# Optimization experiments

Hardware: AMD Instinct MI355X
Metric: run time of the kernel (lower is better)

Reference implementation:

```python
import jax, jax.numpy as jnp
import numpy as np

K = 16  # neighbors (module's self.k)


def _gather(points, idx):
    # points (B,C,N), idx (B,M[,k]) -> (B,C,M[,k])
    return jax.vmap(lambda p, i: p[:, i])(points, idx)


def _fps(xyz, nsample):
    # furthest point sampling on xyz (B,3,N) -> idx (B,nsample) int32
    B, _, N = xyz.shape

    def body(carry, _):
        dists, last = carry
        lp = jnp.take_along_axis(xyz, last[:, None, None], axis=2)  # (B,3,1)
        d = jnp.sum((xyz - lp) ** 2, axis=1)  # (B,N)
        dists = jnp.minimum(dists, d)
        nxt = jnp.argmax(dists, axis=1).astype(jnp.int32)
        return (dists, nxt), nxt

    init_idx = jnp.zeros((B,), dtype=jnp.int32)
    init_d = jnp.full((B, N), jnp.finfo(xyz.dtype).max, xyz.dtype)
    _, rest = jax.lax.scan(body, (init_d, init_idx), None, length=nsample - 1)
    return jnp.concatenate([init_idx[None], rest], axis=0).T  # (B,nsample)


def _knn(query, points, k):
    # query (B,C,M), points (B,C,N): k nearest in feature space
    d = (jnp.sum(query ** 2, axis=1)[:, :, None]
         + jnp.sum(points ** 2, axis=1)[:, None, :]
         - 2.0 * jnp.einsum('bcm,bcn->bmn', query, points))  # (B,M,N)
    _, idx = jax.lax.top_k(-d, k)  # (B,M,k)
    return _gather(points, idx), idx  # (B,C,M,k), (B,M,k)


def _conv1x1(W, b, y):
    # y (B,Cin,M,k), W (Cout,Cin) -> (B,Cout,M,k)
    return jnp.einsum('oi,bimk->bomk', W, y) + b[None, :, None, None]


def setup_inputs() -> dict:
    key = jax.random.key(0)
    ks = jax.random.split(key, 8)
    B, C, N = 4, 64, 8192
    g = 64
    return {
        'x': jax.random.normal(ks[0], (B, C, N), jnp.float32),
        'xyz': jax.random.normal(ks[1], (B, 3, N), jnp.float32),
        'W0': jax.random.normal(ks[2], (g, 2 * C), jnp.float32) * 0.05,
        'b0': jax.random.normal(ks[3], (g,), jnp.float32) * 0.05,
        'W1': jax.random.normal(ks[4], (g, C + g), jnp.float32) * 0.05,
        'b1': jax.random.normal(ks[5], (g,), jnp.float32) * 0.05,
        'W2': jax.random.normal(ks[6], (g, C + 2 * g), jnp.float32) * 0.05,
        'b2': jax.random.normal(ks[7], (g,), jnp.float32) * 0.05,
        'nsample': 2048,
    }


def reference(x, xyz, W0, b0, W1, b1, W2, b2, nsample):
    # furthest point sample on coordinates, gather sampled features
    sampled_idx = _fps(xyz, nsample)              # (B,M)
    sampled_xyz = _gather(xyz, sampled_idx)       # (B,3,M)
    sampled_x = _gather(x, sampled_idx)           # (B,C,M)
    # local graph: k+1 NN in feature space, drop self
    knn_pt, _ = _knn(sampled_x, x, K + 1)
    knn_pt = knn_pt[..., 1:]                      # (B,C,M,K)
    center = sampled_x[..., None]                 # (B,C,M,1)
    center_k = jnp.broadcast_to(center, knn_pt.shape)
    edge = jnp.concatenate([center_k, knn_pt - center_k], axis=1)  # (B,2C,M,K)
    # dense edge conv cascade
    y = jnp.concatenate([jax.nn.relu(_conv1x1(W0, b0, edge)), center_k], axis=1)
    y = jnp.concatenate([jax.nn.relu(_conv1x1(W1, b1, y)), y], axis=1)
    y = jnp.concatenate([_conv1x1(W2, b2, y), y], axis=1)
    y = jnp.max(y, axis=-1)                       # (B, C+3*g, M)
    return (y, sampled_xyz, sampled_idx)
```

## Files before the change

kernel.cpp:

```cpp
#include <hip/hip_runtime.h>
#include <hip/hip_bf16.h>
#include <stdint.h>

typedef unsigned long long u64;
typedef unsigned int u32;
typedef unsigned short u16;

#define B_   4
#define C_   64
#define N_   8192
#define M_   2048
#define KNB  16
#define FLT_MAX_ 3.402823466e+38f

__device__ __forceinline__ int clampN(int v) {
    return v < 0 ? 0 : (v > N_ - 1 ? N_ - 1 : v);
}


__device__ __forceinline__ void pin4(float4& v) {
    asm volatile("" : "+v"(v.x), "+v"(v.y), "+v"(v.z), "+v"(v.w));
}

__device__ __forceinline__ float wave_fmax_dpp(float v) {
    float t;
    t = __int_as_float(__builtin_amdgcn_update_dpp(0, __float_as_int(v), 0x111, 0xf, 0xf, true)); v = fmaxf(v, t);
    t = __int_as_float(__builtin_amdgcn_update_dpp(0, __float_as_int(v), 0x112, 0xf, 0xf, true)); v = fmaxf(v, t);
    t = __int_as_float(__builtin_amdgcn_update_dpp(0, __float_as_int(v), 0x114, 0xf, 0xf, true)); v = fmaxf(v, t);
    t = __int_as_float(__builtin_amdgcn_update_dpp(0, __float_as_int(v), 0x118, 0xf, 0xf, true)); v = fmaxf(v, t);
    t = __int_as_float(__builtin_amdgcn_update_dpp(0, __float_as_int(v), 0x142, 0xa, 0xf, true)); v = fmaxf(v, t);
    t = __int_as_float(__builtin_amdgcn_update_dpp(0, __float_as_int(v), 0x143, 0xc, 0xf, true)); v = fmaxf(v, t);
    return __int_as_float(__builtin_amdgcn_readlane(__float_as_int(v), 63));
}

#define FPS_STEP(PX, PY, PZ, DD, J)                                          \
    {                                                                        \
        float dx = __fsub_rn((PX), lx);                                      \
        float dy = __fsub_rn((PY), ly);                                      \
        float dz = __fsub_rn((PZ), lz);                                      \
        float d = __fadd_rn(__fadd_rn(__fmul_rn(dx, dx), __fmul_rn(dy, dy)), \
                            __fmul_rn(dz, dz));                              \
        float nd = fminf((DD), d);                                           \
        (DD) = nd;                                                           \
        bool gt = nd > fm;                                                   \
        fm = gt ? nd : fm;                                                   \
        fj = gt ? (J) : fj;                                                  \
        fx = gt ? (PX) : fx;                                                 \
        fy = gt ? (PY) : fy;                                                 \
        fz = gt ? (PZ) : fz;                                                 \
    }

__global__ __launch_bounds__(512, 2) void fps_prep_kernel(
    const float* __restrict__ xyz, const float* __restrict__ x,
    const float* __restrict__ W0, const float* __restrict__ W1,
    const float* __restrict__ W2, u16* __restrict__ idx_ws,
    float* __restrict__ pnorm_ws, float* __restrict__ wt,
    float* __restrict__ out1, float* __restrict__ out2) {
    const int bid = blockIdx.x;
    const int tid = threadIdx.x;

    __shared__ float4 red4[2][8];
    __shared__ int    redi[2][8];
    __shared__ u16    hist[M_];

    if (bid >= 64) {
        if (bid < 128) {
            int gid = (bid - 64) * 512 + tid;
            int b = gid >> 13, n = gid & 8191;
            const float* xb = x + b * C_ * N_ + n;
            float acc = 0.f;
#pragma unroll 16
            for (int c = 0; c < C_; ++c) { float v = xb[c * N_]; acc = fmaf(v, v, acc); }
            pnorm_ws[gid] = acc;
        } else {
            int e = (bid - 128) * 512 + tid;
            if (e < 8192) {
                int i = e >> 6, o = e & 63;
                wt[e] = W0[o * 128 + i];
            } else if (e < 16384) {
                int e2 = e - 8192; int i = e2 >> 6, o = e2 & 63;
                wt[8192 + e2] = W1[o * 128 + i];
            } else {
                int e2 = e - 16384; int i = e2 >> 6, o = e2 & 63;
                wt[16384 + e2] = W2[o * 192 + i];
            }
        }
        return;
    }

    const int rep = bid >> 2;
    const int b = bid & 3;
    const int lane = tid & 63;
    const int w = tid >> 6;
    const float* xb = xyz + b * 3 * N_;
    const int n0 = tid * 16;

    float4 px[4], py[4], pz[4], dd[4];
#pragma unroll
    for (int j4 = 0; j4 < 4; ++j4) {
        px[j4] = *(const float4*)(xb + n0 + j4 * 4);
        py[j4] = *(const float4*)(xb + N_ + n0 + j4 * 4);
        pz[j4] = *(const float4*)(xb + 2 * N_ + n0 + j4 * 4);
        pin4(px[j4]); pin4(py[j4]); pin4(pz[j4]);
        dd[j4] = make_float4(FLT_MAX_, FLT_MAX_, FLT_MAX_, FLT_MAX_);
    }

    int cur = 0;
    float lx = xb[0], ly = xb[N_], lz = xb[2 * N_];
    if (tid == 0) { idx_ws[b * M_ + 0] = 0; hist[0] = 0; }

    for (int s = 1; s < M_; ++s) {
        float fm = -1.0f, fx = 0.f, fy = 0.f, fz = 0.f;
        int fj = 0;
#pragma unroll
        for (int j4 = 0; j4 < 4; ++j4) {
            FPS_STEP(px[j4].x, py[j4].x, pz[j4].x, dd[j4].x, j4 * 4 + 0);
            FPS_STEP(px[j4].y, py[j4].y, pz[j4].y, dd[j4].y, j4 * 4 + 1);
            FPS_STEP(px[j4].z, py[j4].z, pz[j4].z, dd[j4].z, j4 * 4 + 2);
            FPS_STEP(px[j4].w, py[j4].w, pz[j4].w, dd[j4].w, j4 * 4 + 3);
        }
        float wm = wave_fmax_dpp(fm);
        u64 bal = __ballot(fm == wm);
        int winlane = (int)__ffsll(bal) - 1;
        const int par = s & 1;
        if (lane == winlane) {
            red4[par][w] = make_float4(wm, fx, fy, fz);
            redi[par][w] = n0 + fj;
        }
        __syncthreads();
        float4 p0 = red4[par][0];
        float g = p0.x; float nlx = p0.y, nly = p0.z, nlz = p0.w;
        int ncur = redi[par][0];
#pragma unroll
        for (int ww = 1; ww < 8; ++ww) {
            float4 p = red4[par][ww];
            int id = redi[par][ww];
            bool gt = p.x > g;
            g = gt ? p.x : g;
            nlx = gt ? p.y : nlx; nly = gt ? p.z : nly; nlz = gt ? p.w : nlz;
            ncur = gt ? id : ncur;
        }
        lx = nlx; ly = nly; lz = nlz; cur = ncur;
        if (tid == 0) { idx_ws[b * M_ + s] = (u16)cur; hist[s] = (u16)cur; }
    }

    __syncthreads();
    if (rep == 0) {
        for (int m = tid; m < M_; m += 512) {
            int idx = (int)hist[m];
            out2[b * M_ + m] = (float)idx;
            out1[(b * 3 + 0) * M_ + m] = xb[idx];
            out1[(b * 3 + 1) * M_ + m] = xb[N_ + idx];
            out1[(b * 3 + 2) * M_ + m] = xb[2 * N_ + idx];
        }
    }
}

__global__ __launch_bounds__(256) void knn_kernel(const float* __restrict__ x,
                                                  const u16* __restrict__ idx_ws,
                                                  const float* __restrict__ pnorm_ws,
                                                  u16* __restrict__ nbr_ws) {
    __shared__ float pt[64 * 68];
    __shared__ float spn[64];
    __shared__ u64 lists[256 * 17];

    const int tid = threadIdx.x;
    const int b = blockIdx.x >> 6;
    const int m0 = (blockIdx.x & 63) * 32;
    const int q = tid & 31, sub = tid >> 5;
    const int m = m0 + q;
    const float* xb = x + b * C_ * N_;
    const int self = clampN((int)idx_ws[b * M_ + m]);

    float4 qv[16];
#pragma unroll
    for (int c4 = 0; c4 < 16; ++c4) {
        qv[c4].x = xb[(c4 * 4 + 0) * N_ + self];
        qv[c4].y = xb[(c4 * 4 + 1) * N_ + self];
        qv[c4].z = xb[(c4 * 4 + 2) * N_ + self];
        qv[c4].w = xb[(c4 * 4 + 3) * N_ + self];
    }
    const float qn = pnorm_ws[b * N_ + self];

    u64* L = lists + tid * 17;
#pragma unroll
    for (int j = 0; j < 17; ++j) L[j] = ~0ULL;
    u64 worst = ~0ULL;

    for (int t = 0; t < N_ / 64; ++t) {
        const int nb0 = t * 64;
        __syncthreads();
#pragma unroll
        for (int r = 0; r < 4; ++r) {
            int e = tid + r * 256;
            int c = e >> 4, nq = e & 15;
            float4 v = *(const float4*)(xb + c * N_ + nb0 + nq * 4);
            const int cs = c ^ (nq << 2);
            pt[(nq * 4 + 0) * 68 + cs] = v.x;
            pt[(nq * 4 + 1) * 68 + cs] = v.y;
            pt[(nq * 4 + 2) * 68 + cs] = v.z;
            pt[(nq * 4 + 3) * 68 + cs] = v.w;
        }
        if (tid < 64) spn[tid] = pnorm_ws[b * N_ + nb0 + tid];
        __syncthreads();
#pragma unroll
        for (int pp = 0; pp < 8; ++pp) {
            int nl = sub * 8 + pp;
            const float* pvbase = pt + nl * 68;
            const int rsw = (nl >> 2) << 2;
            float a0 = 0.f, a1 = 0.f, a2 = 0.f, a3 = 0.f;
#pragma unroll
            for (int c4 = 0; c4 < 16; ++c4) {
                float4 p = *(const float4*)(pvbase + (((c4 << 2) ^ rsw)));
                a0 = fmaf(qv[c4].x, p.x, a0);
                a1 = fmaf(qv[c4].y, p.y, a1);
                a2 = fmaf(qv[c4].z, p.z, a2);
                a3 = fmaf(qv[c4].w, p.w, a3);
            }
            float dot = (a0 + a1) + (a2 + a3);
            float d = qn + spn[nl] - 2.0f * dot;
            u32 db = __float_as_uint(d);
            db = (db & 0x80000000u) ? ~db : (db | 0x80000000u);
            u64 key = ((u64)db << 32) | (u32)(nb0 + nl);
            if (key < worst) {
                int j = 16;
                while (j > 0 && L[j - 1] > key) { L[j] = L[j - 1]; --j; }
                L[j] = key;
                worst = L[16];
            }
        }
    }
    __syncthreads();
    if (tid < 32) {
        int pos[8];
#pragma unroll
        for (int s2 = 0; s2 < 8; ++s2) pos[s2] = 0;
        u16* outp = nbr_ws + (b * M_ + m0 + tid) * KNB;
        for (int r = 0; r < 17; ++r) {
            u64 best = ~0ULL; int bs = 0;
#pragma unroll
            for (int s2 = 0; s2 < 8; ++s2) {
                u64 k2 = (pos[s2] < 17) ? lists[(tid + 32 * s2) * 17 + pos[s2]] : ~0ULL;
                if (k2 < best) { best = k2; bs = s2; }
            }
#pragma unroll
            for (int s2 = 0; s2 < 8; ++s2) pos[s2] += (s2 == bs) ? 1 : 0;
            if (r > 0) outp[r - 1] = (u16)clampN((int)(best & 0xFFFFFFFFu));
        }
    }
}

__device__ __forceinline__ void mm_tile(float a[4][4], const float* __restrict__ w,
                                        const float* __restrict__ s, int ni) {
#pragma unroll 8
    for (int i = 0; i < ni; ++i) {
        const float4 w4 = *(const float4*)(w + i * 64);
        const float4 e4 = *(const float4*)(s + i * 64);
        a[0][0] = fmaf(w4.x, e4.x, a[0][0]);
        a[0][1] = fmaf(w4.x, e4.y, a[0][1]);
        a[0][2] = fmaf(w4.x, e4.z, a[0][2]);
        a[0][3] = fmaf(w4.x, e4.w, a[0][3]);
        a[1][0] = fmaf(w4.y, e4.x, a[1][0]);
        a[1][1] = fmaf(w4.y, e4.y, a[1][1]);
        a[1][2] = fmaf(w4.y, e4.z, a[1][2]);
        a[1][3] = fmaf(w4.y, e4.w, a[1][3]);
        a[2][0] = fmaf(w4.z, e4.x, a[2][0]);
        a[2][1] = fmaf(w4.z, e4.y, a[2][1]);
        a[2][2] = fmaf(w4.z, e4.z, a[2][2]);
        a[2][3] = fmaf(w4.z, e4.w, a[2][3]);
        a[3][0] = fmaf(w4.w, e4.x, a[3][0]);
        a[3][1] = fmaf(w4.w, e4.y, a[3][1]);
        a[3][2] = fmaf(w4.w, e4.z, a[3][2]);
        a[3][3] = fmaf(w4.w, e4.w, a[3][3]);
    }
}

__global__ __launch_bounds__(256) void conv_kernel(const float* __restrict__ x,
                                                   const u16* __restrict__ idx_ws,
                                                   const u16* __restrict__ nbr_ws,
                                                   const float* __restrict__ wt,
                                                   const float* __restrict__ bias0,
                                                   const float* __restrict__ bias1,
                                                   const float* __restrict__ bias2,
                                                   float* __restrict__ out0) {
    __shared__ float E[128 * 64];
    __shared__ float H0[64 * 64];

    const int tid = threadIdx.x;
    const int b = blockIdx.x >> 9;
    const int m0 = (blockIdx.x & 511) * 4;
    const float* xb = x + b * C_ * N_;

    {
        const int col = tid & 63;
        const int half = tid >> 6;
        const int m = m0 + (col >> 4);
        const int k = col & 15;
        const int selfm = clampN((int)idx_ws[b * M_ + m]);
        const int nbr = clampN((int)nbr_ws[(b * M_ + m) * KNB + k]);
#pragma unroll
        for (int c2 = 0; c2 < 16; ++c2) {
            int c = half * 16 + c2;
            float ctr = xb[c * N_ + selfm];
            float nb = xb[c * N_ + nbr];
            E[c * 64 + col] = ctr;
            E[(64 + c) * 64 + col] = __fsub_rn(nb, ctr);
        }
    }
    __syncthreads();

    const int o0 = (tid >> 4) * 4;
    const int c0 = (tid & 15) * 4;
    float a[4][4];

    {
        float4 bb = *(const float4*)(bias0 + o0);
        a[0][0] = a[0][1] = a[0][2] = a[0][3] = bb.x;
        a[1][0] = a[1][1] = a[1][2] = a[1][3] = bb.y;
        a[2][0] = a[2][1] = a[2][2] = a[2][3] = bb.z;
        a[3][0] = a[3][1] = a[3][2] = a[3][3] = bb.w;
        mm_tile(a, wt + o0, E + c0, 128);
#pragma unroll
        for (int oo = 0; oo < 4; ++oo) {
            float4 v = make_float4(fmaxf(a[oo][0], 0.f), fmaxf(a[oo][1], 0.f),
                                   fmaxf(a[oo][2], 0.f), fmaxf(a[oo][3], 0.f));
            *(float4*)(H0 + (o0 + oo) * 64 + c0) = v;
        }
    }
    __syncthreads();

    {
        float4 bb = *(const float4*)(bias1 + o0);
        a[0][0] = a[0][1] = a[0][2] = a[0][3] = bb.x;
        a[1][0] = a[1][1] = a[1][2] = a[1][3] = bb.y;
        a[2][0] = a[2][1] = a[2][2] = a[2][3] = bb.z;
        a[3][0] = a[3][1] = a[3][2] = a[3][3] = bb.w;
        mm_tile(a, wt + 8192 + o0, H0 + c0, 64);
        mm_tile(a, wt + 8192 + 64 * 64 + o0, E + c0, 64);
#pragma unroll
        for (int oo = 0; oo < 4; ++oo) {
            float4 v = make_float4(fmaxf(a[oo][0], 0.f), fmaxf(a[oo][1], 0.f),
                                   fmaxf(a[oo][2], 0.f), fmaxf(a[oo][3], 0.f));
            *(float4*)(E + (64 + o0 + oo) * 64 + c0) = v;
        }
    }
    __syncthreads();

    {
        float4 bb = *(const float4*)(bias2 + o0);
        a[0][0] = a[0][1] = a[0][2] = a[0][3] = bb.x;
        a[1][0] = a[1][1] = a[1][2] = a[1][3] = bb.y;
        a[2][0] = a[2][1] = a[2][2] = a[2][3] = bb.z;
        a[3][0] = a[3][1] = a[3][2] = a[3][3] = bb.w;
        mm_tile(a, wt + 16384 + o0, E + 64 * 64 + c0, 64);
        mm_tile(a, wt + 16384 + 64 * 64 + o0, H0 + c0, 64);
        mm_tile(a, wt + 16384 + 128 * 64 + o0, E + c0, 64);
    }

#pragma unroll
    for (int r = 1; r < 4; ++r) {
        int e = tid + r * 256;
        int ch = e >> 2, mloc = e & 3;
        int colb = mloc * 16;
        float v;
        if (ch < 128) {
            const float* row = E + (64 + (ch - 64)) * 64 + colb;
            v = row[0];
#pragma unroll
            for (int k = 1; k < 16; ++k) v = fmaxf(v, row[k]);
        } else if (ch < 192) {
            const float* row = H0 + (ch - 128) * 64 + colb;
            v = row[0];
#pragma unroll
            for (int k = 1; k < 16; ++k) v = fmaxf(v, row[k]);
        } else {
            v = E[(ch - 192) * 64 + colb];
        }
        out0[((b * 256 + ch) << 11) + m0 + mloc] = v;
    }
    __syncthreads();

    {
#pragma unroll
        for (int oo = 0; oo < 4; ++oo) {
            float4 v = make_float4(a[oo][0], a[oo][1], a[oo][2], a[oo][3]);
            *(float4*)(E + (64 + o0 + oo) * 64 + c0) = v;
        }
    }
    __syncthreads();

    {
        int e = tid;
        int ch = e >> 2, mloc = e & 3;
        int colb = mloc * 16;
        const float* row = E + (64 + ch) * 64 + colb;
        float v = row[0];
#pragma unroll
        for (int k = 1; k < 16; ++k) v = fmaxf(v, row[k]);
        out0[((b * 256 + ch) << 11) + m0 + mloc] = v;
    }
}

extern "C" void kernel_launch(void* const* d_in, const int* in_sizes, int n_in,
                              void* d_out, int out_size, void* d_ws, size_t ws_size,
                              hipStream_t stream) {
    const float* x   = (const float*)d_in[0];
    const float* xyz = (const float*)d_in[1];
    const float* W0  = (const float*)d_in[2];
    const float* b0  = (const float*)d_in[3];
    const float* W1  = (const float*)d_in[4];
    const float* b1  = (const float*)d_in[5];
    const float* W2  = (const float*)d_in[6];
    const float* b2  = (const float*)d_in[7];

    float* out  = (float*)d_out;
    float* out0 = out;
    float* out1 = out + 4 * 256 * 2048;
    float* out2 = out1 + 4 * 3 * 2048;

    char* ws = (char*)d_ws;
    u16*   idx_ws   = (u16*)ws;
    u16*   nbr_ws   = (u16*)(ws + 16384);
    float* pnorm_ws = (float*)(ws + 278528);
    float* wt_ws    = (float*)(ws + 409600);

    fps_prep_kernel<<<184, 512, 0, stream>>>(xyz, x, W0, W1, W2,
                                             idx_ws, pnorm_ws, wt_ws, out1, out2);
    knn_kernel<<<256, 256, 0, stream>>>(x, idx_ws, pnorm_ws, nbr_ws);
    conv_kernel<<<2048, 256, 0, stream>>>(x, idx_ws, nbr_ws, wt_ws, b0, b1, b2, out0);
}
```

Before: 2.969 ms.

## Fuse FPS and KNN into one persistent kernel with flag-based streaming

Measured after the change: 3.432 ms. 1.16x slower.

```diff
diff --git a/kernel.cpp b/kernel.cpp
--- a/kernel.cpp
+++ b/kernel.cpp
@@ -12,6 +12,7 @@
 #define M_   2048
 #define KNB  16
 #define FLT_MAX_ 3.402823466e+38f
+#define SMEM_SZ 86016
 
 __device__ __forceinline__ int clampN(int v) {
     return v < 0 ? 0 : (v > N_ - 1 ? N_ - 1 : v);
@@ -50,202 +51,227 @@
         fz = gt ? (PZ) : fz;                                                 \
     }
 
-__global__ __launch_bounds__(512, 2) void fps_prep_kernel(
+__global__ void init_kernel(u32* __restrict__ flags) {
+    if (threadIdx.x < 16) flags[threadIdx.x] = 0;
+}
+
+__global__ __launch_bounds__(256, 1) void mega_kernel(
     const float* __restrict__ xyz, const float* __restrict__ x,
     const float* __restrict__ W0, const float* __restrict__ W1,
     const float* __restrict__ W2, u16* __restrict__ idx_ws,
     float* __restrict__ pnorm_ws, float* __restrict__ wt,
-    float* __restrict__ out1, float* __restrict__ out2) {
+    float* __restrict__ out1, float* __restrict__ out2,
+    u16* __restrict__ nbr_ws, u32* __restrict__ flags) {
     const int bid = blockIdx.x;
     const int tid = threadIdx.x;
-
-    __shared__ float4 red4[2][8];
-    __shared__ int    redi[2][8];
-    __shared__ u16    hist[M_];
-
-    if (bid >= 64) {
-        if (bid < 128) {
-            int gid = (bid - 64) * 512 + tid;
-            int b = gid >> 13, n = gid & 8191;
-            const float* xb = x + b * C_ * N_ + n;
-            float acc = 0.f;
-#pragma unroll 16
-            for (int c = 0; c < C_; ++c) { float v = xb[c * N_]; acc = fmaf(v, v, acc); }
-            pnorm_ws[gid] = acc;
-        } else {
-            int e = (bid - 128) * 512 + tid;
-            if (e < 8192) {
-                int i = e >> 6, o = e & 63;
-                wt[e] = W0[o * 128 + i];
-            } else if (e < 16384) {
-                int e2 = e - 8192; int i = e2 >> 6, o = e2 & 63;
-                wt[8192 + e2] = W1[o * 128 + i];
-            } else {
-                int e2 = e - 16384; int i = e2 >> 6, o = e2 & 63;
-                wt[16384 + e2] = W2[o * 192 + i];
-            }
-        }
-        return;
-    }
-
-    const int rep = bid >> 2;
-    const int b = bid & 3;
-    const int lane = tid & 63;
-    const int w = tid >> 6;
-    const float* xb = xyz + b * 3 * N_;
-    const int n0 = tid * 16;
-
-    float4 px[4], py[4], pz[4], dd[4];
-#pragma unroll
-    for (int j4 = 0; j4 < 4; ++j4) {
-        px[j4] = *(const float4*)(xb + n0 + j4 * 4);
-        py[j4] = *(const float4*)(xb + N_ + n0 + j4 * 4);
-        pz[j4] = *(const float4*)(xb + 2 * N_ + n0 + j4 * 4);
-        pin4(px[j4]); pin4(py[j4]); pin4(pz[j4]);
-        dd[j4] = make_float4(FLT_MAX_, FLT_MAX_, FLT_MAX_, FLT_MAX_);
-    }
-
-    int cur = 0;
-    float lx = xb[0], ly = xb[N_], lz = xb[2 * N_];
-    if (tid == 0) { idx_ws[b * M_ + 0] = 0; hist[0] = 0; }
-
-    for (int s = 1; s < M_; ++s) {
-        float fm = -1.0f, fx = 0.f, fy = 0.f, fz = 0.f;
-        int fj = 0;
-#pragma unroll
-        for (int j4 = 0; j4 < 4; ++j4) {
-            FPS_STEP(px[j4].x, py[j4].x, pz[j4].x, dd[j4].x, j4 * 4 + 0);
-            FPS_STEP(px[j4].y, py[j4].y, pz[j4].y, dd[j4].y, j4 * 4 + 1);
-            FPS_STEP(px[j4].z, py[j4].z, pz[j4].z, dd[j4].z, j4 * 4 + 2);
-            FPS_STEP(px[j4].w, py[j4].w, pz[j4].w, dd[j4].w, j4 * 4 + 3);
-        }
-        float wm = wave_fmax_dpp(fm);
-        u64 bal = __ballot(fm == wm);
-        int winlane = (int)__ffsll(bal) - 1;
-        const int par = s & 1;
-        if (lane == winlane) {
-            red4[par][w] = make_float4(wm, fx, fy, fz);
-            redi[par][w] = n0 + fj;
-        }
+    __shared__ __align__(16) char SM[SMEM_SZ];
+
+    if (bid < 4) {
+        const int b = bid;
+        const int lane = tid & 63;
+        const int w = tid >> 6;
+        const float* xb = xyz + b * 3 * N_;
+        const int n0 = tid * 32;
+
+        float4* red4 = (float4*)SM;
+        int*    redi = (int*)(SM + 128);
+        u16*    hist = (u16*)(SM + 160);
+
+        float4 px[8], py[8], pz[8], dd[8];
+#pragma unroll
+        for (int j4 = 0; j4 < 8; ++j4) {
+            px[j4] = *(const float4*)(xb + n0 + j4 * 4);
+            py[j4] = *(const float4*)(xb + N_ + n0 + j4 * 4);
+            pz[j4] = *(const float4*)(xb + 2 * N_ + n0 + j4 * 4);
+            pin4(px[j4]); pin4(py[j4]); pin4(pz[j4]);
+            dd[j4] = make_float4(FLT_MAX_, FLT_MAX_, FLT_MAX_, FLT_MAX_);
+        }
+
+        int cur = 0;
+        float lx = xb[0], ly = xb[N_], lz = xb[2 * N_];
+        if (tid == 0) { idx_ws[b * M_ + 0] = 0; hist[0] = 0; }
+
+        for (int s = 1; s < M_; ++s) {
+            float fm = -1.0f, fx = 0.f, fy = 0.f, fz = 0.f;
+            int fj = 0;
+#pragma unroll
+            for (int j4 = 0; j4 < 8; ++j4) {
+                FPS_STEP(px[j4].x, py[j4].x, pz[j4].x, dd[j4].x, j4 * 4 + 0);
+                FPS_STEP(px[j4].y, py[j4].y, pz[j4].y, dd[j4].y, j4 * 4 + 1);
+                FPS_STEP(px[j4].z, py[j4].z, pz[j4].z, dd[j4].z, j4 * 4 + 2);
+                FPS_STEP(px[j4].w, py[j4].w, pz[j4].w, dd[j4].w, j4 * 4 + 3);
+            }
+            float wm = wave_fmax_dpp(fm);
+            u64 bal = __ballot(fm == wm);
+            int winlane = (int)__ffsll(bal) - 1;
+            const int par = s & 1;
+            if (lane == winlane) {
+                red4[(par << 2) + w] = make_float4(wm, fx, fy, fz);
+                redi[(par << 2) + w] = n0 + fj;
+            }
+            __syncthreads();
+            float4 p0 = red4[par << 2];
+            float g = p0.x; float nlx = p0.y, nly = p0.z, nlz = p0.w;
+            int ncur = redi[par << 2];
+#pragma unroll
+            for (int ww = 1; ww < 4; ++ww) {
+                float4 p = red4[(par << 2) + ww];
+                int id = redi[(par << 2) + ww];
+                bool gt = p.x > g;
+                g = gt ? p.x : g;
+                nlx = gt ? p.y : nlx; nly = gt ? p.z : nly; nlz = gt ? p.w : nlz;
+                ncur = gt ? id : ncur;
+            }
+            lx = nlx; ly = nly; lz = nlz; cur = ncur;
+            if (tid == 0) {
+                idx_ws[b * M_ + s] = (u16)cur; hist[s] = (u16)cur;
+                if ((s & 63) == 63)
+                    __hip_atomic_store(&flags[b], (u32)s, __ATOMIC_RELEASE,
+                                       __HIP_MEMORY_SCOPE_AGENT);
+            }
+        }
+
         __syncthreads();
-        float4 p0 = red4[par][0];
-        float g = p0.x; float nlx = p0.y, nly = p0.z, nlz = p0.w;
-        int ncur = redi[par][0];
-#pragma unroll
-        for (int ww = 1; ww < 8; ++ww) {
-            float4 p = red4[par][ww];
-            int id = redi[par][ww];
-            bool gt = p.x > g;
-            g = gt ? p.x : g;
-            nlx = gt ? p.y : nlx; nly = gt ? p.z : nly; nlz = gt ? p.w : nlz;
-            ncur = gt ? id : ncur;
-        }
-        lx = nlx; ly = nly; lz = nlz; cur = ncur;
-        if (tid == 0) { idx_ws[b * M_ + s] = (u16)cur; hist[s] = (u16)cur; }
-    }
-
-    __syncthreads();
-    if (rep == 0) {
-        for (int m = tid; m < M_; m += 512) {
+        for (int m = tid; m < M_; m += 256) {
             int idx = (int)hist[m];
             out2[b * M_ + m] = (float)idx;
             out1[(b * 3 + 0) * M_ + m] = xb[idx];
             out1[(b * 3 + 1) * M_ + m] = xb[N_ + idx];
             out1[(b * 3 + 2) * M_ + m] = xb[2 * N_ + idx];
         }
-    }
-}
-
-__global__ __launch_bounds__(256) void knn_kernel(const float* __restrict__ x,
-                                                  const u16* __restrict__ idx_ws,
-                                                  const float* __restrict__ pnorm_ws,
-                                                  u16* __restrict__ nbr_ws) {
-    __shared__ float pt[64 * 68];
-    __shared__ float spn[64];
-    __shared__ u64 lists[256 * 17];
-
-    const int tid = threadIdx.x;
-    const int b = blockIdx.x >> 6;
-    const int m0 = (blockIdx.x & 63) * 32;
-    const int q = tid & 31, sub = tid >> 5;
-    const int m = m0 + q;
-    const float* xb = x + b * C_ * N_;
-    const int self = clampN((int)idx_ws[b * M_ + m]);
-
-    float4 qv[16];
-#pragma unroll
-    for (int c4 = 0; c4 < 16; ++c4) {
-        qv[c4].x = xb[(c4 * 4 + 0) * N_ + self];
-        qv[c4].y = xb[(c4 * 4 + 1) * N_ + self];
-        qv[c4].z = xb[(c4 * 4 + 2) * N_ + self];
-        qv[c4].w = xb[(c4 * 4 + 3) * N_ + self];
-    }
-    const float qn = pnorm_ws[b * N_ + self];
-
-    u64* L = lists + tid * 17;
-#pragma unroll
-    for (int j = 0; j < 17; ++j) L[j] = ~0ULL;
-    u64 worst = ~0ULL;
-
-    for (int t = 0; t < N_ / 64; ++t) {
-        const int nb0 = t * 64;
+        return;
+    }
+
+    if (bid < 132) {
+        int gid = (bid - 4) * 256 + tid;
+        int bb = gid >> 13, n = gid & 8191;
+        const float* xb = x + bb * C_ * N_ + n;
+        float acc = 0.f;
+#pragma unroll 16
+        for (int c = 0; c < C_; ++c) { float v = xb[c * N_]; acc = fmaf(v, v, acc); }
+        pnorm_ws[gid] = acc;
         __syncthreads();
-#pragma unroll
-        for (int r = 0; r < 4; ++r) {
-            int e = tid + r * 256;
-            int c = e >> 4, nq = e & 15;
-            float4 v = *(const float4*)(xb + c * N_ + nb0 + nq * 4);
-            const int cs = c ^ (nq << 2);
-            pt[(nq * 4 + 0) * 68 + cs] = v.x;
-            pt[(nq * 4 + 1) * 68 + cs] = v.y;
-            pt[(nq * 4 + 2) * 68 + cs] = v.z;
-            pt[(nq * 4 + 3) * 68 + cs] = v.w;
-        }
-        if (tid < 64) spn[tid] = pnorm_ws[b * N_ + nb0 + tid];
+        if (tid == 0)
+            __hip_atomic_fetch_add(&flags[4], 1u, __ATOMIC_RELEASE,
+                                   __HIP_MEMORY_SCOPE_AGENT);
+        return;
+    }
+
+    if (bid < 244) {
+        int e = (bid - 132) * 256 + tid;
+        if (e < 8192) {
+            int i = e >> 6, o = e & 63;
+            wt[e] = W0[o * 128 + i];
+        } else if (e < 16384) {
+            int e2 = e - 8192; int i = e2 >> 6, o = e2 & 63;
+            wt[8192 + e2] = W1[o * 128 + i];
+        } else {
+            int e2 = e - 16384; int i = e2 >> 6, o = e2 & 63;
+            wt[16384 + e2] = W2[o * 192 + i];
+        }
+        return;
+    }
+
+    {
+        const int kid = bid - 244;
+        const int b = kid >> 6;
+        const int m0 = (kid & 63) * 32;
+
+        float* pt    = (float*)SM;
+        float* spn   = (float*)(SM + 17408);
+        u64*   lists = (u64*)(SM + 17664);
+
+        if (tid == 0) {
+            while (__hip_atomic_load(&flags[4], __ATOMIC_ACQUIRE,
+                                     __HIP_MEMORY_SCOPE_AGENT) < 128u)
+                __builtin_amdgcn_s_sleep(2);
+            const u32 need = (u32)(m0 + 31);
+            while (__hip_atomic_load(&flags[b], __ATOMIC_ACQUIRE,
+                                     __HIP_MEMORY_SCOPE_AGENT) < need)
+                __builtin_amdgcn_s_sleep(2);
+        }
         __syncthreads();
-#pragma unroll
-        for (int pp = 0; pp < 8; ++pp) {
-            int nl = sub * 8 + pp;
-            const float* pvbase = pt + nl * 68;
-            const int rsw = (nl >> 2) << 2;
-            float a0 = 0.f, a1 = 0.f, a2 = 0.f, a3 = 0.f;
-#pragma unroll
-            for (int c4 = 0; c4 < 16; ++c4) {
-                float4 p = *(const float4*)(pvbase + (((c4 << 2) ^ rsw)));
-                a0 = fmaf(qv[c4].x, p.x, a0);
-                a1 = fmaf(qv[c4].y, p.y, a1);
-                a2 = fmaf(qv[c4].z, p.z, a2);
-                a3 = fmaf(qv[c4].w, p.w, a3);
-            }
-            float dot = (a0 + a1) + (a2 + a3);
-            float d = qn + spn[nl] - 2.0f * dot;
-            u32 db = __float_as_uint(d);
-            db = (db & 0x80000000u) ? ~db : (db | 0x80000000u);
-            u64 key = ((u64)db << 32) | (u32)(nb0 + nl);
-            if (key < worst) {
-                int j = 16;
-                while (j > 0 && L[j - 1] > key) { L[j] = L[j - 1]; --j; }
-                L[j] = key;
-                worst = L[16];
-            }
-        }
-    }
-    __syncthreads();
-    if (tid < 32) {
-        int pos[8];
-#pragma unroll
-        for (int s2 = 0; s2 < 8; ++s2) pos[s2] = 0;
-        u16* outp = nbr_ws + (b * M_ + m0 + tid) * KNB;
-        for (int r = 0; r < 17; ++r) {
-            u64 best = ~0ULL; int bs = 0;
-#pragma unroll
-            for (int s2 = 0; s2 < 8; ++s2) {
-                u64 k2 = (pos[s2] < 17) ? lists[(tid + 32 * s2) * 17 + pos[s2]] : ~0ULL;
-                if (k2 < best) { best = k2; bs = s2; }
-            }
-#pragma unroll
-            for (int s2 = 0; s2 < 8; ++s2) pos[s2] += (s2 == bs) ? 1 : 0;
-            if (r > 0) outp[r - 1] = (u16)clampN((int)(best & 0xFFFFFFFFu));
+
+        const int q = tid & 31, sub = tid >> 5;
+        const int m = m0 + q;
+        const float* xb = x + b * C_ * N_;
+        const int self = clampN((int)idx_ws[b * M_ + m]);
+
+        float4 qv[16];
+#pragma unroll
+        for (int c4 = 0; c4 < 16; ++c4) {
+            qv[c4].x = xb[(c4 * 4 + 0) * N_ + self];
+            qv[c4].y = xb[(c4 * 4 + 1) * N_ + self];
+            qv[c4].z = xb[(c4 * 4 + 2) * N_ + self];
+            qv[c4].w = xb[(c4 * 4 + 3) * N_ + self];
+        }
+        const float qn = pnorm_ws[b * N_ + self];
+
+        u64* L = lists + tid * 17;
+#pragma unroll
+        for (int j = 0; j < 17; ++j) L[j] = ~0ULL;
+        u64 worst = ~0ULL;
+
+        for (int t = 0; t < N_ / 64; ++t) {
+            const int nb0 = t * 64;
+            __syncthreads();
+#pragma unroll
+            for (int r = 0; r < 4; ++r) {
+                int e = tid + r * 256;
+                int c = e >> 4, nq = e & 15;
+                float4 v = *(const float4*)(xb + c * N_ + nb0 + nq * 4);
+                const int cs = c ^ (nq << 2);
+                pt[(nq * 4 + 0) * 68 + cs] = v.x;
+                pt[(nq * 4 + 1) * 68 + cs] = v.y;
+                pt[(nq * 4 + 2) * 68 + cs] = v.z;
+                pt[(nq * 4 + 3) * 68 + cs] = v.w;
+            }
+            if (tid < 64) spn[tid] = pnorm_ws[b * N_ + nb0 + tid];
+            __syncthreads();
+#pragma unroll
+            for (int pp = 0; pp < 8; ++pp) {
+                int nl = sub * 8 + pp;
+                const float* pvbase = pt + nl * 68;
+                const int rsw = (nl >> 2) << 2;
+                float a0 = 0.f, a1 = 0.f, a2 = 0.f, a3 = 0.f;
+#pragma unroll
+                for (int c4 = 0; c4 < 16; ++c4) {
+                    float4 p = *(const float4*)(pvbase + (((c4 << 2) ^ rsw)));
+                    a0 = fmaf(qv[c4].x, p.x, a0);
+                    a1 = fmaf(qv[c4].y, p.y, a1);
+                    a2 = fmaf(qv[c4].z, p.z, a2);
+                    a3 = fmaf(qv[c4].w, p.w, a3);
+                }
+                float dot = (a0 + a1) + (a2 + a3);
+                float d = qn + spn[nl] - 2.0f * dot;
+                u32 db = __float_as_uint(d);
+                db = (db & 0x80000000u) ? ~db : (db | 0x80000000u);
+                u64 key = ((u64)db << 32) | (u32)(nb0 + nl);
+                if (key < worst) {
+                    int j = 16;
+                    while (j > 0 && L[j - 1] > key) { L[j] = L[j - 1]; --j; }
+                    L[j] = key;
+                    worst = L[16];
+                }
+            }
+        }
+        __syncthreads();
+        if (tid < 32) {
+            int pos[8];
+#pragma unroll
+            for (int s2 = 0; s2 < 8; ++s2) pos[s2] = 0;
+            u16* outp = nbr_ws + (b * M_ + m0 + tid) * KNB;
+            for (int r = 0; r < 17; ++r) {
+                u64 best = ~0ULL; int bs = 0;
+#pragma unroll
+                for (int s2 = 0; s2 < 8; ++s2) {
+                    u64 k2 = (pos[s2] < 17) ? lists[(tid + 32 * s2) * 17 + pos[s2]] : ~0ULL;
+                    if (k2 < best) { best = k2; bs = s2; }
+                }
+#pragma unroll
+                for (int s2 = 0; s2 < 8; ++s2) pos[s2] += (s2 == bs) ? 1 : 0;
+                if (r > 0) outp[r - 1] = (u16)clampN((int)(best & 0xFFFFFFFFu));
+            }
         }
     }
 }
@@ -390,8 +416,7 @@
     __syncthreads();
 
     {
-        int e = tid;
-        int ch = e >> 2, mloc = e & 3;
+        int ch = tid >> 2, mloc = tid & 3;
         int colb = mloc * 16;
         const float* row = E + (64 + ch) * 64 + colb;
         float v = row[0];
@@ -417,6 +442,7 @@
     float* out0 = out;
     float* out1 = out + 4 * 256 * 2048;
     float* out2 = out1 + 4 * 3 * 2048;
+    u32*   flags = (u32*)out0;
 
     char* ws = (char*)d_ws;
     u16*   idx_ws   = (u16*)ws;
@@ -424,8 +450,10 @@
     float* pnorm_ws = (float*)(ws + 278528);
     float* wt_ws    = (float*)(ws + 409600);
 
-    fps_prep_kernel<<<184, 512, 0, stream>>>(xyz, x, W0, W1, W2,
-                                             idx_ws, pnorm_ws, wt_ws, out1, out2);
-    knn_kernel<<<256, 256, 0, stream>>>(x, idx_ws, pnorm_ws, nbr_ws);
-    conv_kernel<<<2048, 256, 0, stream>>>(x, idx_ws, nbr_ws, wt_ws, b0, b1, b2, out0);
-}
+    init_kernel<<<1, 64, 0, stream>>>(flags);
+    mega_kernel<<<500, 256, 0, stream>>>(xyz, x, W0, W1, W2,
+                                         idx_ws, pnorm_ws, wt_ws,
+                                         out1, out2, nbr_ws, flags);
+    conv_kernel<<<2048, 256, 0, stream>>>(x, idx_ws, nbr_ws, wt_ws,
+                                          b0, b1, b2, out0);
+}
```
